# Optimization experiments

Measured on AMD Instinct MI355X. Metric: run time of the kernel, lower is better.

The kernel has to match this reference:

```python
import jax, jax.numpy as jnp
import numpy as np
from functools import partial

H = 768
E = 1536
B = 4
L = 4096

def layer_norm(x, g, b, eps=1e-5):
    mu = jnp.mean(x, axis=-1, keepdims=True)
    var = jnp.mean((x - mu) ** 2, axis=-1, keepdims=True)
    return (x - mu) * jax.lax.rsqrt(var + eps) * g + b

def l2_normalize(x, eps=1e-12):
    n = jnp.sqrt(jnp.sum(x * x, axis=-1, keepdims=True))
    return x / jnp.maximum(n, eps)

def dw_conv(x, w):
    # x: [B, L, E], w: [E, 1, 3] depthwise kernel (torch Conv1d groups=E layout)
    y = jax.lax.conv_general_dilated(
        x.transpose(0, 2, 1), w, window_strides=(1,), padding=[(1, 1)],
        dimension_numbers=('NCH', 'OIH', 'NCH'), feature_group_count=E)
    return y.transpose(0, 2, 1)

def setup_inputs() -> dict:
    key = jax.random.key(0)
    ks = jax.random.split(key, 12)
    d = {}
    d['x'] = jax.random.normal(ks[0], (B, L, H), jnp.float32)
    d['ln1_g'] = jnp.ones((H,), jnp.float32)
    d['ln1_b'] = jnp.zeros((H,), jnp.float32)
    d['ln2_g'] = jnp.ones((E,), jnp.float32)
    d['ln2_b'] = jnp.zeros((E,), jnp.float32)
    d['W_in'] = 0.02 * jax.random.normal(ks[1], (3 * E, H), jnp.float32)
    d['b_in'] = jnp.zeros((3 * E,), jnp.float32)
    d['W_beta'] = jnp.zeros((E, H), jnp.float32)  # torch init: constant 0
    d['b_beta'] = jnp.ones((E,), jnp.float32)     # torch init: constant 1
    d['W_out'] = 0.02 * jax.random.normal(ks[2], (H, E), jnp.float32)
    d['b_out'] = jnp.zeros((H,), jnp.float32)
    d['W1'] = 0.02 * jax.random.normal(ks[3], (4 * H, H), jnp.float32)
    d['b1'] = jnp.zeros((4 * H,), jnp.float32)
    d['W2'] = 0.02 * jax.random.normal(ks[4], (H, 4 * H), jnp.float32)
    d['b2'] = jnp.zeros((H,), jnp.float32)
    d['conv_w'] = jax.random.normal(ks[5], (E, 1, 3), jnp.float32) / jnp.sqrt(3.0)
    d['attn_scale'] = jnp.ones((1,), jnp.float32)
    return d

def reference(x, ln1_g, ln1_b, ln2_g, ln2_b, W_in, b_in, W_beta, b_beta,
              W_out, b_out, W1, b1, W2, b2, conv_w, attn_scale):
    shortcut = x
    xn = layer_norm(x, ln1_g, ln1_b)
    qkv = xn @ W_in.T + b_in
    q, k, v = jnp.split(qkv, 3, axis=-1)
    q = jax.nn.silu(q)
    k = jax.nn.silu(k)
    v = jax.nn.gelu(v, approximate=False)
    q = l2_normalize(q) + 0.1 * k
    k = l2_normalize(k) + 0.1 * q
    q = dw_conv(q, conv_w)
    k = dw_conv(k, conv_w)
    v = dw_conv(v, conv_w)
    beta = jax.nn.sigmoid(xn @ W_beta.T + b_beta) * 0.9 + 0.1
    # initial state is zero, so v_old = 0 and v_new = beta * v (same math as torch code)
    v_new = beta * v                                   # [B, L, E]
    state = jnp.einsum('ble,blf->bef', v_new, k)       # v_new^T @ k : [B, E, E]
    out = jnp.einsum('blf,bef->ble', q, state)         # q @ state^T
    out = out * attn_scale
    out = layer_norm(out, ln2_g, ln2_b)
    out = out @ W_out.T + b_out
    x = shortcut + out
    h = layer_norm(x, ln1_g, ln1_b)
    h = jax.nn.gelu(h @ W1.T + b1, approximate=False) @ W2.T + b2
    return x + h
```

## Files before the change

### kernel.cpp

```cpp
#include <hip/hip_runtime.h>
#include <hip/hip_bf16.h>
#include <cstdint>
#include <cstddef>

using bf16_t = __hip_bfloat16;
typedef __bf16 bf16x8 __attribute__((ext_vector_type(8)));
typedef __bf16 bf16x4 __attribute__((ext_vector_type(4)));
typedef float f32x4 __attribute__((ext_vector_type(4)));

#define DEVI static __device__ __forceinline__

DEVI float b2f(bf16_t v) { return __bfloat162float(v); }

DEVI float fsigmoid(float x) { return 1.0f / (1.0f + __expf(-x)); }
DEVI float fsilu(float x) { return x * fsigmoid(x); }
DEVI float fgelu(float x) { return 0.5f * x * (1.0f + erff(x * 0.70710678118654752440f)); }

DEVI void g2l16(const bf16_t* g, bf16_t* l) {
    __builtin_amdgcn_global_load_lds(
        (const __attribute__((address_space(1))) void*)g,
        (__attribute__((address_space(3))) void*)l,
        16, 0, 0);
}

template<int ACT, bool RESID, bool OUTBF, bool QKVSPLIT>
__global__ __launch_bounds__(256) void gemm_nt(
    const bf16_t* __restrict__ A, const bf16_t* __restrict__ B,
    void* __restrict__ Cout, const float* __restrict__ bias,
    const float* __restrict__ resid,
    int M, int N, int K, long long sA, long long sB, long long sC)
{
    __shared__ bf16_t As[128 * 64];
    __shared__ bf16_t Bs[128 * 64];

    const int t  = threadIdx.x;
    const int w  = t >> 6;
    const int ln = t & 63;
    const long long bz = blockIdx.z;
    A += bz * sA;
    B += bz * sB;
    const long long cbase = QKVSPLIT ? 0 : bz * sC;

    const int m0 = blockIdx.y * 128;
    const int n0 = blockIdx.x * 128;
    const int wm = (w >> 1) * 64;
    const int wn = (w & 1) * 64;

    f32x4 acc[4][4] = {};

    const int sr = ln >> 3;
    const int sc = (ln & 7) ^ sr;
    const bf16_t* Ap = A + (size_t)(m0 + w * 32 + sr) * K + sc * 8;
    const bf16_t* Bp = B + (size_t)(n0 + w * 32 + sr) * K + sc * 8;
    bf16_t* ldsA = &As[(w * 32) * 64];
    bf16_t* ldsB = &Bs[(w * 32) * 64];

    const int fr = ln & 15;
    const int qd = ln >> 4;
    int roA[4], roB[4];
#pragma unroll
    for (int i = 0; i < 4; ++i) {
        roA[i] = (wm + i * 16 + fr) * 64;
        roB[i] = (wn + i * 16 + fr) * 64;
    }
    const int so0 = ((qd)     ^ (fr & 7)) * 8;
    const int so1 = ((4 + qd) ^ (fr & 7)) * 8;

    for (int k0 = 0; k0 < K; k0 += 64) {
#pragma unroll
        for (int i = 0; i < 4; ++i) {
            g2l16(Ap + (size_t)(i * 8) * K, ldsA + (i * 8) * 64);
            g2l16(Bp + (size_t)(i * 8) * K, ldsB + (i * 8) * 64);
        }
        Ap += 64; Bp += 64;
        __syncthreads();

        bf16x8 af[4], bfr[4];
#pragma unroll
        for (int i = 0; i < 4; ++i) {
            af[i]  = *(const bf16x8*)&As[roA[i] + so0];
            bfr[i] = *(const bf16x8*)&Bs[roB[i] + so0];
        }
#pragma unroll
        for (int mi = 0; mi < 4; ++mi)
#pragma unroll
            for (int ni = 0; ni < 4; ++ni)
                acc[mi][ni] = __builtin_amdgcn_mfma_f32_16x16x32_bf16(
                    bfr[ni], af[mi], acc[mi][ni], 0, 0, 0);
#pragma unroll
        for (int i = 0; i < 4; ++i) {
            af[i]  = *(const bf16x8*)&As[roA[i] + so1];
            bfr[i] = *(const bf16x8*)&Bs[roB[i] + so1];
        }
#pragma unroll
        for (int mi = 0; mi < 4; ++mi)
#pragma unroll
            for (int ni = 0; ni < 4; ++ni)
                acc[mi][ni] = __builtin_amdgcn_mfma_f32_16x16x32_bf16(
                    bfr[ni], af[mi], acc[mi][ni], 0, 0, 0);
        __syncthreads();
    }

    const int rb = qd * 4;
    const int seg = QKVSPLIT ? (n0 / 1536) : 0;
    f32x4 bias4[4];
#pragma unroll
    for (int ni = 0; ni < 4; ++ni) {
        f32x4 z = {};
        bias4[ni] = bias ? *(const f32x4*)&bias[n0 + wn + ni * 16 + rb] : z;
    }
#pragma unroll
    for (int mi = 0; mi < 4; ++mi) {
        const int row = m0 + wm + mi * 16 + fr;
#pragma unroll
        for (int ni = 0; ni < 4; ++ni) {
            const int col0 = n0 + wn + ni * 16 + rb;
            f32x4 v = acc[mi][ni] + bias4[ni];
            if constexpr (ACT == 1) {
#pragma unroll
                for (int r = 0; r < 4; ++r) v[r] = fgelu(v[r]);
            }
            if constexpr (ACT == 3) {
                if (seg <= 1) {
#pragma unroll
                    for (int r = 0; r < 4; ++r) v[r] = fsilu(v[r]);
                } else if (seg == 2) {
#pragma unroll
                    for (int r = 0; r < 4; ++r) v[r] = fgelu(v[r]);
                } else {
#pragma unroll
                    for (int r = 0; r < 4; ++r) v[r] = fsigmoid(v[r]) * 0.9f + 0.1f;
                }
            }
            long long off;
            if constexpr (QKVSPLIT) {
                off = (long long)seg * sC + (long long)row * 1536
                    + (col0 - seg * 1536);
            } else {
                off = cbase + (long long)row * N + col0;
            }
            if constexpr (RESID) v += *(const f32x4*)&resid[off];
            if constexpr (OUTBF) {
                bf16x4 o;
#pragma unroll
                for (int r = 0; r < 4; ++r) o[r] = (__bf16)v[r];
                *(bf16x4*)((bf16_t*)Cout + off) = o;
            } else {
                *(f32x4*)((float*)Cout + off) = v;
            }
        }
    }
}

template<int NT>
__global__ __launch_bounds__(NT) void ln_v4(
    const float* __restrict__ x, const float* __restrict__ g,
    const float* __restrict__ b, bf16_t* __restrict__ out)
{
    constexpr int n = NT * 4;
    constexpr int NW = NT / 64;
    const int row = blockIdx.x, t = threadIdx.x;
    f32x4 v = *(const f32x4*)&x[(size_t)row * n + t * 4];
    float s  = v[0] + v[1] + v[2] + v[3];
    float ss = v[0]*v[0] + v[1]*v[1] + v[2]*v[2] + v[3]*v[3];
#pragma unroll
    for (int m = 32; m; m >>= 1) { s += __shfl_xor(s, m, 64); ss += __shfl_xor(ss, m, 64); }
    __shared__ float red[2 * NW];
    const int w = t >> 6;
    if ((t & 63) == 0) { red[w] = s; red[NW + w] = ss; }
    __syncthreads();
    s = 0.f; ss = 0.f;
#pragma unroll
    for (int i = 0; i < NW; ++i) { s += red[i]; ss += red[NW + i]; }
    const float mean = s / n;
    const float rstd = rsqrtf(ss / n - mean * mean + 1e-5f);
    const f32x4 gv = *(const f32x4*)&g[t * 4];
    const f32x4 bv = *(const f32x4*)&b[t * 4];
    bf16x4 o;
#pragma unroll
    for (int r = 0; r < 4; ++r)
        o[r] = (__bf16)((v[r] - mean) * rstd * gv[r] + bv[r]);
    *(bf16x4*)&out[(size_t)row * n + t * 4] = o;
}

__global__ __launch_bounds__(192) void ln_bf16_1536(
    const bf16_t* __restrict__ x, const float* __restrict__ g,
    const float* __restrict__ b, bf16_t* __restrict__ out,
    const float* __restrict__ scale_ptr)
{
    const int row = blockIdx.x, t = threadIdx.x;
    const float scale = scale_ptr[0];
    const bf16x8 x8 = *(const bf16x8*)&x[(size_t)row * 1536 + t * 8];
    float v[8];
    float s = 0.f, ss = 0.f;
#pragma unroll
    for (int i = 0; i < 8; ++i) {
        v[i] = (float)x8[i] * scale;
        s += v[i]; ss += v[i] * v[i];
    }
#pragma unroll
    for (int m = 32; m; m >>= 1) { s += __shfl_xor(s, m, 64); ss += __shfl_xor(ss, m, 64); }
    __shared__ float red[6];
    const int w = t >> 6;
    if ((t & 63) == 0) { red[w] = s; red[3 + w] = ss; }
    __syncthreads();
    s  = red[0] + red[1] + red[2];
    ss = red[3] + red[4] + red[5];
    const float mean = s / 1536.f;
    const float rstd = rsqrtf(ss / 1536.f - mean * mean + 1e-5f);
    const f32x4 g0 = *(const f32x4*)&g[t * 8];
    const f32x4 g1 = *(const f32x4*)&g[t * 8 + 4];
    const f32x4 b0 = *(const f32x4*)&b[t * 8];
    const f32x4 b1 = *(const f32x4*)&b[t * 8 + 4];
    bf16x8 o;
#pragma unroll
    for (int r = 0; r < 4; ++r) {
        o[r]     = (__bf16)((v[r]     - mean) * rstd * g0[r] + b0[r]);
        o[r + 4] = (__bf16)((v[r + 4] - mean) * rstd * g1[r] + b1[r]);
    }
    *(bf16x8*)&out[(size_t)row * 1536 + t * 8] = o;
}

__global__ __launch_bounds__(192) void qk_norms(
    const bf16_t* __restrict__ q, const bf16_t* __restrict__ k,
    float2* __restrict__ norms)
{
    const int row = blockIdx.x, t = threadIdx.x;
    const bf16x8 q8 = *(const bf16x8*)&q[(size_t)row * 1536 + t * 8];
    const bf16x8 k8 = *(const bf16x8*)&k[(size_t)row * 1536 + t * 8];
    float sq = 0.f, sk = 0.f;
#pragma unroll
    for (int i = 0; i < 8; ++i) {
        const float a = (float)q8[i];
        const float c = (float)k8[i];
        sq += a * a; sk += c * c;
    }
#pragma unroll
    for (int m = 32; m; m >>= 1) { sq += __shfl_xor(sq, m, 64); sk += __shfl_xor(sk, m, 64); }
    __shared__ float red[6];
    const int w = t >> 6;
    if ((t & 63) == 0) { red[w] = sq; red[3 + w] = sk; }
    __syncthreads();
    if (t == 0) {
        sq = red[0] + red[1] + red[2];
        sk = red[3] + red[4] + red[5];
        float2 o;
        o.x = 1.0f / fmaxf(sqrtf(sq), 1e-12f);
        o.y = 1.0f / fmaxf(sqrtf(sk), 1e-12f);
        norms[row] = o;
    }
}

__global__ __launch_bounds__(256) void ac_qk(
    const bf16_t* __restrict__ qs, const bf16_t* __restrict__ ks,
    const float2* __restrict__ norms,
    bf16_t* __restrict__ qc, bf16_t* __restrict__ kT,
    const float* __restrict__ cw)
{
    constexpr int L = 4096, E = 1536;
    const int b = blockIdx.z;
    const int e0 = blockIdx.x * 64, l0 = blockIdx.y * 64;
    const int t = threadIdx.x;
    const int e = e0 + (t & 15) * 4;
    const int lbase = l0 + (t >> 4) * 4;
    const size_t rowL = (size_t)b * L;

    float w0[4], w1[4], w2[4];
#pragma unroll
    for (int i = 0; i < 4; ++i) {
        w0[i] = cw[(e + i) * 3 + 0];
        w1[i] = cw[(e + i) * 3 + 1];
        w2[i] = cw[(e + i) * 3 + 2];
    }

    float sq[6][4], sk[6][4];
#pragma unroll
    for (int j = 0; j < 6; ++j) {
        const int l = lbase - 1 + j;
        if (l < 0 || l >= L) {
#pragma unroll
            for (int i = 0; i < 4; ++i) { sq[j][i] = 0.f; sk[j][i] = 0.f; }
            continue;
        }
        const size_t off = (rowL + l) * E + e;
        const bf16x4 q4 = *(const bf16x4*)&qs[off];
        const bf16x4 k4 = *(const bf16x4*)&ks[off];
        const float2 nm = norms[rowL + l];
#pragma unroll
        for (int i = 0; i < 4; ++i) {
            const float q1 = (float)q4[i] * nm.x + 0.1f * (float)k4[i];
            const float k1 = (float)k4[i] * nm.y + 0.1f * q1;
            sq[j][i] = q1; sk[j][i] = k1;
        }
    }

#pragma unroll
    for (int j = 0; j < 4; ++j) {
        bf16x4 oq;
#pragma unroll
        for (int i = 0; i < 4; ++i)
            oq[i] = (__bf16)(w0[i] * sq[j][i] + w1[i] * sq[j + 1][i] + w2[i] * sq[j + 2][i]);
        *(bf16x4*)&qc[(rowL + lbase + j) * E + e] = oq;
    }
#pragma unroll
    for (int i = 0; i < 4; ++i) {
        bf16x4 ok;
#pragma unroll
        for (int j = 0; j < 4; ++j)
            ok[j] = (__bf16)(w0[i] * sk[j][i] + w1[i] * sk[j + 1][i] + w2[i] * sk[j + 2][i]);
        *(bf16x4*)&kT[((size_t)b * E + e + i) * L + lbase] = ok;
    }
}

__global__ __launch_bounds__(256) void ac_v(
    const bf16_t* __restrict__ vg, const bf16_t* __restrict__ beta,
    bf16_t* __restrict__ vT, const float* __restrict__ cw)
{
    constexpr int L = 4096, E = 1536;
    const int b = blockIdx.z;
    const int e0 = blockIdx.x * 64, l0 = blockIdx.y * 64;
    const int t = threadIdx.x;
    const int e = e0 + (t & 15) * 4;
    const int lbase = l0 + (t >> 4) * 4;
    const size_t rowL = (size_t)b * L;

    float w0[4], w1[4], w2[4];
#pragma unroll
    for (int i = 0; i < 4; ++i) {
        w0[i] = cw[(e + i) * 3 + 0];
        w1[i] = cw[(e + i) * 3 + 1];
        w2[i] = cw[(e + i) * 3 + 2];
    }

    float s[6][4];
#pragma unroll
    for (int j = 0; j < 6; ++j) {
        const int l = lbase - 1 + j;
        if (l < 0 || l >= L) {
#pragma unroll
            for (int i = 0; i < 4; ++i) s[j][i] = 0.f;
            continue;
        }
        const bf16x4 v4 = *(const bf16x4*)&vg[(rowL + l) * E + e];
#pragma unroll
        for (int i = 0; i < 4; ++i) s[j][i] = (float)v4[i];
    }

    float o[4][4];
#pragma unroll
    for (int j = 0; j < 4; ++j) {
        const bf16x4 b4 = *(const bf16x4*)&beta[(rowL + lbase + j) * E + e];
#pragma unroll
        for (int i = 0; i < 4; ++i)
            o[j][i] = (w0[i] * s[j][i] + w1[i] * s[j + 1][i] + w2[i] * s[j + 2][i])
                      * (float)b4[i];
    }
#pragma unroll
    for (int i = 0; i < 4; ++i) {
        bf16x4 ov;
#pragma unroll
        for (int j = 0; j < 4; ++j) ov[j] = (__bf16)o[j][i];
        *(bf16x4*)&vT[((size_t)b * E + e + i) * L + lbase] = ov;
    }
}

__global__ __launch_bounds__(256) void prep1(
    const float* __restrict__ Win, const float* __restrict__ Wbeta,
    const float* __restrict__ bin, const float* __restrict__ bbeta,
    bf16_t* __restrict__ Wcat, float* __restrict__ bcat)
{
    constexpr int nWin4 = 3 * 1536 * 768 / 4;
    constexpr int nWb4  = 1536 * 768 / 4;
    const int i = blockIdx.x * 256 + threadIdx.x;
    if (i < nWin4) {
        const f32x4 v = ((const f32x4*)Win)[i];
        bf16x4 o;
#pragma unroll
        for (int r = 0; r < 4; ++r) o[r] = (__bf16)v[r];
        ((bf16x4*)Wcat)[i] = o;
    } else if (i < nWin4 + nWb4) {
        const f32x4 v = ((const f32x4*)Wbeta)[i - nWin4];
        bf16x4 o;
#pragma unroll
        for (int r = 0; r < 4; ++r) o[r] = (__bf16)v[r];
        ((bf16x4*)Wcat)[i] = o;
    } else {
        const int j = i - nWin4 - nWb4;
        ((f32x4*)bcat)[j] = (j < 1152) ? ((const f32x4*)bin)[j]
                                       : ((const f32x4*)bbeta)[j - 1152];
    }
}

__global__ __launch_bounds__(256) void prep2(
    const float* __restrict__ Wout, const float* __restrict__ W1,
    const float* __restrict__ W2, bf16_t* __restrict__ dst)
{
    constexpr int n0 = 768 * 1536 / 4;
    constexpr int n1 = n0 + 3072 * 768 / 4;
    const int i = blockIdx.x * 256 + threadIdx.x;
    const float* src;
    int j;
    if (i < n0)      { src = Wout; j = i; }
    else if (i < n1) { src = W1;   j = i - n0; }
    else             { src = W2;   j = i - n1; }
    const f32x4 v = ((const f32x4*)src)[j];
    bf16x4 o;
#pragma unroll
    for (int r = 0; r < 4; ++r) o[r] = (__bf16)v[r];
    ((bf16x4*)dst)[i] = o;
}

__global__ void diag_ws(float* o, float v) { o[threadIdx.x] = v; }


extern "C" void kernel_launch(void* const* d_in, const int* in_sizes, int n_in,
                              void* d_out, int out_size, void* d_ws, size_t ws_size,
                              hipStream_t stream)
{
    constexpr int B = 4, L = 4096, H = 768, E = 1536;
    constexpr int T = B * L;
    constexpr size_t SEGE = (size_t)T * E;
    constexpr size_t S    = SEGE * 2;
    constexpr size_t o_bcat  = 5 * S;
    constexpr size_t o_norms = o_bcat + 6144 * 4;
    constexpr size_t WS_NEED = o_norms + (size_t)T * 8;

    const float* x       = (const float*)d_in[0];
    const float* ln1_g   = (const float*)d_in[1];
    const float* ln1_b   = (const float*)d_in[2];
    const float* ln2_g   = (const float*)d_in[3];
    const float* ln2_b   = (const float*)d_in[4];
    const float* W_in    = (const float*)d_in[5];
    const float* b_in    = (const float*)d_in[6];
    const float* W_beta  = (const float*)d_in[7];
    const float* b_beta  = (const float*)d_in[8];
    const float* W_out   = (const float*)d_in[9];
    const float* b_out   = (const float*)d_in[10];
    const float* W1      = (const float*)d_in[11];
    const float* b1      = (const float*)d_in[12];
    const float* W2      = (const float*)d_in[13];
    const float* b2      = (const float*)d_in[14];
    const float* conv_w  = (const float*)d_in[15];
    const float* attn_sc = (const float*)d_in[16];

    if (ws_size < WS_NEED) {
        diag_ws<<<1, 256, 0, stream>>>((float*)d_out,
                                       10000.0f + (float)(ws_size >> 20));
        return;
    }

    char* ws = (char*)d_ws;
    bf16_t* slotA = (bf16_t*)(ws + 0 * S);
    bf16_t* slotB = (bf16_t*)(ws + 1 * S);
    bf16_t* slotC = (bf16_t*)(ws + 2 * S);
    bf16_t* slotD = (bf16_t*)(ws + 3 * S);
    bf16_t* slotE = (bf16_t*)(ws + 4 * S);
    float*  bcat  = (float*)(ws + o_bcat);
    float2* norms = (float2*)(ws + o_norms);

    bf16_t* Wcat = slotE;
    bf16_t* xn   = (bf16_t*)((char*)slotE + (size_t)6144 * H * 2);

    bf16_t* vT    = slotE;
    bf16_t* kT    = slotC;
    bf16_t* qc    = slotD;
    bf16_t* state = slotA;
    bf16_t* WoutB = (bf16_t*)((char*)slotA + (size_t)20 * 1024 * 1024);
    bf16_t* W1B   = WoutB + (size_t)H * E;
    bf16_t* W2B   = W1B + (size_t)4 * H * H;
    bf16_t* attn  = slotB;
    bf16_t* ln2o  = slotE;
    float*  x2    = (float*)slotC;
    bf16_t* xn2   = slotB;
    bf16_t* h1    = slotD;

    prep1<<<4614, 256, 0, stream>>>(W_in, W_beta, b_in, b_beta, Wcat, bcat);

    ln_v4<192><<<T, 192, 0, stream>>>(x, ln1_g, ln1_b, xn);

    gemm_nt<3, false, true, true><<<dim3(6144 / 128, T / 128, 1), 256, 0, stream>>>(
        xn, Wcat, slotA, bcat, nullptr, T, 6144, H, 0, 0, (long long)SEGE);

    qk_norms<<<T, 192, 0, stream>>>(slotA, slotB, norms);

    ac_v <<<dim3(E / 64, L / 64, B), 256, 0, stream>>>(slotC, slotD, vT, conv_w);
    ac_qk<<<dim3(E / 64, L / 64, B), 256, 0, stream>>>(slotA, slotB, norms, qc, kT, conv_w);

    prep2<<<5760, 256, 0, stream>>>(W_out, W1, W2, WoutB);

    gemm_nt<0, false, true, false><<<dim3(E / 128, E / 128, B), 256, 0, stream>>>(
        vT, kT, state, nullptr, nullptr, E, E, L,
        (long long)E * L, (long long)E * L, (long long)E * E);

    gemm_nt<0, false, true, false><<<dim3(E / 128, L / 128, B), 256, 0, stream>>>(
        qc, state, attn, nullptr, nullptr, L, E, E,
        (long long)L * E, (long long)E * E, (long long)L * E);

    ln_bf16_1536<<<T, 192, 0, stream>>>(attn, ln2_g, ln2_b, ln2o, attn_sc);

    gemm_nt<0, true, false, false><<<dim3(H / 128, T / 128, 1), 256, 0, stream>>>(
        ln2o, WoutB, x2, b_out, x, T, H, E, 0, 0, 0);

    ln_v4<192><<<T, 192, 0, stream>>>(x2, ln1_g, ln1_b, xn2);

    gemm_nt<1, false, true, false><<<dim3(4 * H / 128, T / 128, 1), 256, 0, stream>>>(
        xn2, W1B, h1, b1, nullptr, T, 4 * H, H, 0, 0, 0);

    gemm_nt<0, true, false, false><<<dim3(H / 128, T / 128, 1), 256, 0, stream>>>(
        h1, W2B, (float*)d_out, b2, x2, T, H, 4 * H, 0, 0, 0);
}
```

Measured before the change: 1.090 ms.

## Switch GEMM to 32x32x16 MFMA with 32-wide K tiles

```diff
diff --git a/kernel.cpp b/kernel.cpp
--- a/kernel.cpp
+++ b/kernel.cpp
@@ -7,6 +7,7 @@
 typedef __bf16 bf16x8 __attribute__((ext_vector_type(8)));
 typedef __bf16 bf16x4 __attribute__((ext_vector_type(4)));
 typedef float f32x4 __attribute__((ext_vector_type(4)));
+typedef float f32x16 __attribute__((ext_vector_type(16)));
 
 #define DEVI static __device__ __forceinline__
 
@@ -30,8 +31,8 @@
     const float* __restrict__ resid,
     int M, int N, int K, long long sA, long long sB, long long sC)
 {
-    __shared__ bf16_t As[128 * 64];
-    __shared__ bf16_t Bs[128 * 64];
+    __shared__ bf16_t As[128 * 32];
+    __shared__ bf16_t Bs[128 * 32];
 
     const int t  = threadIdx.x;
     const int w  = t >> 6;
@@ -46,107 +47,106 @@
     const int wm = (w >> 1) * 64;
     const int wn = (w & 1) * 64;
 
-    f32x4 acc[4][4] = {};
-
-    const int sr = ln >> 3;
-    const int sc = (ln & 7) ^ sr;
-    const bf16_t* Ap = A + (size_t)(m0 + w * 32 + sr) * K + sc * 8;
-    const bf16_t* Bp = B + (size_t)(n0 + w * 32 + sr) * K + sc * 8;
-    bf16_t* ldsA = &As[(w * 32) * 64];
-    bf16_t* ldsB = &Bs[(w * 32) * 64];
-
-    const int fr = ln & 15;
-    const int qd = ln >> 4;
-    int roA[4], roB[4];
-#pragma unroll
-    for (int i = 0; i < 4; ++i) {
-        roA[i] = (wm + i * 16 + fr) * 64;
-        roB[i] = (wn + i * 16 + fr) * 64;
-    }
-    const int so0 = ((qd)     ^ (fr & 7)) * 8;
-    const int so1 = ((4 + qd) ^ (fr & 7)) * 8;
-
-    for (int k0 = 0; k0 < K; k0 += 64) {
-#pragma unroll
-        for (int i = 0; i < 4; ++i) {
-            g2l16(Ap + (size_t)(i * 8) * K, ldsA + (i * 8) * 64);
-            g2l16(Bp + (size_t)(i * 8) * K, ldsB + (i * 8) * 64);
+    f32x16 acc[2][2] = {};
+
+    const int rI0 = (w * 2 + 0) * 16 + (ln >> 2);
+    const int rI1 = (w * 2 + 1) * 16 + (ln >> 2);
+    const int kc8 = (((ln & 3) ^ ((ln >> 3) & 3)) * 8);
+    bf16_t* ldsA0 = &As[(w * 2 + 0) * 512];
+    bf16_t* ldsA1 = &As[(w * 2 + 1) * 512];
+    bf16_t* ldsB0 = &Bs[(w * 2 + 0) * 512];
+    bf16_t* ldsB1 = &Bs[(w * 2 + 1) * 512];
+
+    const int r32 = ln & 31;
+    const int h   = ln >> 5;
+    const int sw  = (r32 >> 1) & 3;
+    const int offK0 = ((h)     ^ sw) * 8;
+    const int offK1 = ((2 + h) ^ sw) * 8;
+    int roA[2], roB[2];
+#pragma unroll
+    for (int i = 0; i < 2; ++i) {
+        roA[i] = (wm + i * 32 + r32) * 32;
+        roB[i] = (wn + i * 32 + r32) * 32;
+    }
+
+    for (int k0 = 0; k0 < K; k0 += 32) {
+        g2l16(A + (size_t)(m0 + rI0) * K + k0 + kc8, ldsA0);
+        g2l16(A + (size_t)(m0 + rI1) * K + k0 + kc8, ldsA1);
+        g2l16(B + (size_t)(n0 + rI0) * K + k0 + kc8, ldsB0);
+        g2l16(B + (size_t)(n0 + rI1) * K + k0 + kc8, ldsB1);
+        __syncthreads();
+
+        bf16x8 af[2], bfr[2];
+#pragma unroll
+        for (int i = 0; i < 2; ++i) {
+            af[i]  = *(const bf16x8*)&As[roA[i] + offK0];
+            bfr[i] = *(const bf16x8*)&Bs[roB[i] + offK0];
         }
-        Ap += 64; Bp += 64;
-        __syncthreads();
-
-        bf16x8 af[4], bfr[4];
-#pragma unroll
-        for (int i = 0; i < 4; ++i) {
-            af[i]  = *(const bf16x8*)&As[roA[i] + so0];
-            bfr[i] = *(const bf16x8*)&Bs[roB[i] + so0];
+#pragma unroll
+        for (int mi = 0; mi < 2; ++mi)
+#pragma unroll
+            for (int ni = 0; ni < 2; ++ni)
+                acc[mi][ni] = __builtin_amdgcn_mfma_f32_32x32x16_bf16(
+                    bfr[ni], af[mi], acc[mi][ni], 0, 0, 0);
+#pragma unroll
+        for (int i = 0; i < 2; ++i) {
+            af[i]  = *(const bf16x8*)&As[roA[i] + offK1];
+            bfr[i] = *(const bf16x8*)&Bs[roB[i] + offK1];
         }
 #pragma unroll
-        for (int mi = 0; mi < 4; ++mi)
-#pragma unroll
-            for (int ni = 0; ni < 4; ++ni)
-                acc[mi][ni] = __builtin_amdgcn_mfma_f32_16x16x32_bf16(
-                    bfr[ni], af[mi], acc[mi][ni], 0, 0, 0);
-#pragma unroll
-        for (int i = 0; i < 4; ++i) {
-            af[i]  = *(const bf16x8*)&As[roA[i] + so1];
-            bfr[i] = *(const bf16x8*)&Bs[roB[i] + so1];
-        }
-#pragma unroll
-        for (int mi = 0; mi < 4; ++mi)
-#pragma unroll
-            for (int ni = 0; ni < 4; ++ni)
-                acc[mi][ni] = __builtin_amdgcn_mfma_f32_16x16x32_bf16(
+        for (int mi = 0; mi < 2; ++mi)
+#pragma unroll
+            for (int ni = 0; ni < 2; ++ni)
+                acc[mi][ni] = __builtin_amdgcn_mfma_f32_32x32x16_bf16(
                     bfr[ni], af[mi], acc[mi][ni], 0, 0, 0);
         __syncthreads();
     }
 
-    const int rb = qd * 4;
     const int seg = QKVSPLIT ? (n0 / 1536) : 0;
-    f32x4 bias4[4];
-#pragma unroll
-    for (int ni = 0; ni < 4; ++ni) {
-        f32x4 z = {};
-        bias4[ni] = bias ? *(const f32x4*)&bias[n0 + wn + ni * 16 + rb] : z;
-    }
-#pragma unroll
-    for (int mi = 0; mi < 4; ++mi) {
-        const int row = m0 + wm + mi * 16 + fr;
-#pragma unroll
-        for (int ni = 0; ni < 4; ++ni) {
-            const int col0 = n0 + wn + ni * 16 + rb;
-            f32x4 v = acc[mi][ni] + bias4[ni];
-            if constexpr (ACT == 1) {
-#pragma unroll
-                for (int r = 0; r < 4; ++r) v[r] = fgelu(v[r]);
-            }
-            if constexpr (ACT == 3) {
-                if (seg <= 1) {
-#pragma unroll
-                    for (int r = 0; r < 4; ++r) v[r] = fsilu(v[r]);
-                } else if (seg == 2) {
+#pragma unroll
+    for (int mi = 0; mi < 2; ++mi) {
+        const int row = m0 + wm + mi * 32 + r32;
+#pragma unroll
+        for (int ni = 0; ni < 2; ++ni) {
+#pragma unroll
+            for (int g = 0; g < 4; ++g) {
+                const int col0 = n0 + wn + ni * 32 + 8 * g + 4 * h;
+                f32x4 v;
+#pragma unroll
+                for (int r = 0; r < 4; ++r) v[r] = acc[mi][ni][4 * g + r];
+                if (bias) v += *(const f32x4*)&bias[col0];
+                if constexpr (ACT == 1) {
 #pragma unroll
                     for (int r = 0; r < 4; ++r) v[r] = fgelu(v[r]);
+                }
+                if constexpr (ACT == 3) {
+                    if (seg <= 1) {
+#pragma unroll
+                        for (int r = 0; r < 4; ++r) v[r] = fsilu(v[r]);
+                    } else if (seg == 2) {
+#pragma unroll
+                        for (int r = 0; r < 4; ++r) v[r] = fgelu(v[r]);
+                    } else {
+#pragma unroll
+                        for (int r = 0; r < 4; ++r) v[r] = fsigmoid(v[r]) * 0.9f + 0.1f;
+                    }
+                }
+                long long off;
+                if constexpr (QKVSPLIT) {
+                    off = (long long)seg * sC + (long long)row * 1536
+                        + (col0 - seg * 1536);
                 } else {
-#pragma unroll
-                    for (int r = 0; r < 4; ++r) v[r] = fsigmoid(v[r]) * 0.9f + 0.1f;
+                    off = cbase + (long long)row * N + col0;
                 }
-            }
-            long long off;
-            if constexpr (QKVSPLIT) {
-                off = (long long)seg * sC + (long long)row * 1536
-                    + (col0 - seg * 1536);
-            } else {
-                off = cbase + (long long)row * N + col0;
-            }
-            if constexpr (RESID) v += *(const f32x4*)&resid[off];
-            if constexpr (OUTBF) {
-                bf16x4 o;
-#pragma unroll
-                for (int r = 0; r < 4; ++r) o[r] = (__bf16)v[r];
-                *(bf16x4*)((bf16_t*)Cout + off) = o;
-            } else {
-                *(f32x4*)((float*)Cout + off) = v;
+                if constexpr (RESID) v += *(const f32x4*)&resid[off];
+                if constexpr (OUTBF) {
+                    bf16x4 o;
+#pragma unroll
+                    for (int r = 0; r < 4; ++r) o[r] = (__bf16)v[r];
+                    *(bf16x4*)((bf16_t*)Cout + off) = o;
+                } else {
+                    *(f32x4*)((float*)Cout + off) = v;
+                }
             }
         }
     }
```

Result: slower. 1.125 ms (+3.2%).

## Fuse q/k squared-norm reduction into QKV GEMM epilogue and use fast erf

Applied to the files above, without the earlier changes.

```diff
diff --git a/kernel.cpp b/kernel.cpp
--- a/kernel.cpp
+++ b/kernel.cpp
@@ -14,7 +14,18 @@
 
 DEVI float fsigmoid(float x) { return 1.0f / (1.0f + __expf(-x)); }
 DEVI float fsilu(float x) { return x * fsigmoid(x); }
-DEVI float fgelu(float x) { return 0.5f * x * (1.0f + erff(x * 0.70710678118654752440f)); }
+
+DEVI float ferf(float x) {
+    const float ax = fabsf(x);
+    const float t = 1.0f / fmaf(0.3275911f, ax, 1.0f);
+    float p = fmaf(1.061405429f, t, -1.453152027f);
+    p = fmaf(p, t, 1.421413741f);
+    p = fmaf(p, t, -0.284496736f);
+    p = fmaf(p, t, 0.254829592f);
+    p = p * t * __expf(-ax * ax);
+    return copysignf(1.0f - p, x);
+}
+DEVI float fgelu(float x) { return 0.5f * x * (1.0f + ferf(x * 0.70710678118654752440f)); }
 
 DEVI void g2l16(const bf16_t* g, bf16_t* l) {
     __builtin_amdgcn_global_load_lds(
@@ -28,6 +39,7 @@
     const bf16_t* __restrict__ A, const bf16_t* __restrict__ B,
     void* __restrict__ Cout, const float* __restrict__ bias,
     const float* __restrict__ resid,
+    float* __restrict__ normq, float* __restrict__ normk,
     int M, int N, int K, long long sA, long long sB, long long sC)
 {
     __shared__ bf16_t As[128 * 64];
@@ -112,6 +124,7 @@
 #pragma unroll
     for (int mi = 0; mi < 4; ++mi) {
         const int row = m0 + wm + mi * 16 + fr;
+        float s2 = 0.f;
 #pragma unroll
         for (int ni = 0; ni < 4; ++ni) {
             const int col0 = n0 + wn + ni * 16 + rb;
@@ -124,6 +137,7 @@
                 if (seg <= 1) {
 #pragma unroll
                     for (int r = 0; r < 4; ++r) v[r] = fsilu(v[r]);
+                    s2 += v[0]*v[0] + v[1]*v[1] + v[2]*v[2] + v[3]*v[3];
                 } else if (seg == 2) {
 #pragma unroll
                     for (int r = 0; r < 4; ++r) v[r] = fgelu(v[r]);
@@ -147,6 +161,14 @@
                 *(bf16x4*)((bf16_t*)Cout + off) = o;
             } else {
                 *(f32x4*)((float*)Cout + off) = v;
+            }
+        }
+        if constexpr (ACT == 3) {
+            if (seg <= 1) {
+                s2 += __shfl_xor(s2, 16, 64);
+                s2 += __shfl_xor(s2, 32, 64);
+                if (qd == 0)
+                    atomicAdd((seg == 0 ? normq : normk) + row, s2);
             }
         }
     }
@@ -221,39 +243,9 @@
     *(bf16x8*)&out[(size_t)row * 1536 + t * 8] = o;
 }
 
-__global__ __launch_bounds__(192) void qk_norms(
-    const bf16_t* __restrict__ q, const bf16_t* __restrict__ k,
-    float2* __restrict__ norms)
-{
-    const int row = blockIdx.x, t = threadIdx.x;
-    const bf16x8 q8 = *(const bf16x8*)&q[(size_t)row * 1536 + t * 8];
-    const bf16x8 k8 = *(const bf16x8*)&k[(size_t)row * 1536 + t * 8];
-    float sq = 0.f, sk = 0.f;
-#pragma unroll
-    for (int i = 0; i < 8; ++i) {
-        const float a = (float)q8[i];
-        const float c = (float)k8[i];
-        sq += a * a; sk += c * c;
-    }
-#pragma unroll
-    for (int m = 32; m; m >>= 1) { sq += __shfl_xor(sq, m, 64); sk += __shfl_xor(sk, m, 64); }
-    __shared__ float red[6];
-    const int w = t >> 6;
-    if ((t & 63) == 0) { red[w] = sq; red[3 + w] = sk; }
-    __syncthreads();
-    if (t == 0) {
-        sq = red[0] + red[1] + red[2];
-        sk = red[3] + red[4] + red[5];
-        float2 o;
-        o.x = 1.0f / fmaxf(sqrtf(sq), 1e-12f);
-        o.y = 1.0f / fmaxf(sqrtf(sk), 1e-12f);
-        norms[row] = o;
-    }
-}
-
 __global__ __launch_bounds__(256) void ac_qk(
     const bf16_t* __restrict__ qs, const bf16_t* __restrict__ ks,
-    const float2* __restrict__ norms,
+    const float* __restrict__ nq, const float* __restrict__ nk,
     bf16_t* __restrict__ qc, bf16_t* __restrict__ kT,
     const float* __restrict__ cw)
 {
@@ -285,11 +277,12 @@
         const size_t off = (rowL + l) * E + e;
         const bf16x4 q4 = *(const bf16x4*)&qs[off];
         const bf16x4 k4 = *(const bf16x4*)&ks[off];
-        const float2 nm = norms[rowL + l];
+        const float rq = 1.0f / fmaxf(sqrtf(nq[rowL + l]), 1e-12f);
+        const float rk = 1.0f / fmaxf(sqrtf(nk[rowL + l]), 1e-12f);
 #pragma unroll
         for (int i = 0; i < 4; ++i) {
-            const float q1 = (float)q4[i] * nm.x + 0.1f * (float)k4[i];
-            const float k1 = (float)k4[i] * nm.y + 0.1f * q1;
+            const float q1 = (float)q4[i] * rq + 0.1f * (float)k4[i];
+            const float k1 = (float)k4[i] * rk + 0.1f * q1;
             sq[j][i] = q1; sk[j][i] = k1;
         }
     }
@@ -456,7 +449,8 @@
     bf16_t* slotD = (bf16_t*)(ws + 3 * S);
     bf16_t* slotE = (bf16_t*)(ws + 4 * S);
     float*  bcat  = (float*)(ws + o_bcat);
-    float2* norms = (float2*)(ws + o_norms);
+    float*  nq    = (float*)(ws + o_norms);
+    float*  nk    = nq + T;
 
     bf16_t* Wcat = slotE;
     bf16_t* xn   = (bf16_t*)((char*)slotE + (size_t)6144 * H * 2);
@@ -474,38 +468,37 @@
     bf16_t* xn2   = slotB;
     bf16_t* h1    = slotD;
 
+    hipMemsetAsync(nq, 0, (size_t)T * 2 * sizeof(float), stream);
     prep1<<<4614, 256, 0, stream>>>(W_in, W_beta, b_in, b_beta, Wcat, bcat);
 
     ln_v4<192><<<T, 192, 0, stream>>>(x, ln1_g, ln1_b, xn);
 
     gemm_nt<3, false, true, true><<<dim3(6144 / 128, T / 128, 1), 256, 0, stream>>>(
-        xn, Wcat, slotA, bcat, nullptr, T, 6144, H, 0, 0, (long long)SEGE);
-
-    qk_norms<<<T, 192, 0, stream>>>(slotA, slotB, norms);
+        xn, Wcat, slotA, bcat, nullptr, nq, nk, T, 6144, H, 0, 0, (long long)SEGE);
 
     ac_v <<<dim3(E / 64, L / 64, B), 256, 0, stream>>>(slotC, slotD, vT, conv_w);
-    ac_qk<<<dim3(E / 64, L / 64, B), 256, 0, stream>>>(slotA, slotB, norms, qc, kT, conv_w);
+    ac_qk<<<dim3(E / 64, L / 64, B), 256, 0, stream>>>(slotA, slotB, nq, nk, qc, kT, conv_w);
 
     prep2<<<5760, 256, 0, stream>>>(W_out, W1, W2, WoutB);
 
     gemm_nt<0, false, true, false><<<dim3(E / 128, E / 128, B), 256, 0, stream>>>(
-        vT, kT, state, nullptr, nullptr, E, E, L,
+        vT, kT, state, nullptr, nullptr, nullptr, nullptr, E, E, L,
         (long long)E * L, (long long)E * L, (long long)E * E);
 
     gemm_nt<0, false, true, false><<<dim3(E / 128, L / 128, B), 256, 0, stream>>>(
-        qc, state, attn, nullptr, nullptr, L, E, E,
+        qc, state, attn, nullptr, nullptr, nullptr, nullptr, L, E, E,
         (long long)L * E, (long long)E * E, (long long)L * E);
 
     ln_bf16_1536<<<T, 192, 0, stream>>>(attn, ln2_g, ln2_b, ln2o, attn_sc);
 
     gemm_nt<0, true, false, false><<<dim3(H / 128, T / 128, 1), 256, 0, stream>>>(
-        ln2o, WoutB, x2, b_out, x, T, H, E, 0, 0, 0);
+        ln2o, WoutB, x2, b_out, x, nullptr, nullptr, T, H, E, 0, 0, 0);
 
     ln_v4<192><<<T, 192, 0, stream>>>(x2, ln1_g, ln1_b, xn2);
 
     gemm_nt<1, false, true, false><<<dim3(4 * H / 128, T / 128, 1), 256, 0, stream>>>(
-        xn2, W1B, h1, b1, nullptr, T, 4 * H, H, 0, 0, 0);
+        xn2, W1B, h1, b1, nullptr, nullptr, nullptr, T, 4 * H, H, 0, 0, 0);
 
     gemm_nt<0, true, false, false><<<dim3(H / 128, T / 128, 1), 256, 0, stream>>>(
-        h1, W2B, (float*)d_out, b2, x2, T, H, 4 * H, 0, 0, 0);
-}
+        h1, W2B, (float*)d_out, b2, x2, nullptr, nullptr, T, H, 4 * H, 0, 0, 0);
+}
```

Result: faster. 1.003 ms (-8.0%).
